# Optimization experiments

Measured on AMD Instinct MI355X. Metric: run time of the kernel, lower is better.

The kernel has to match this reference:

```python
import jax, jax.numpy as jnp
import numpy as np

B, N, M, D, F, H = 8, 512, 512, 512, 512, 8
D_H, F_H = D // H, F // H


def setup_inputs() -> dict:
    key = jax.random.key(0)
    ks = jax.random.split(key, 7)
    X = jax.random.normal(ks[0], (B, N, D), dtype=jnp.float32)
    V = jax.random.normal(ks[1], (B, M, F), dtype=jnp.float32)
    # learned parameters, init normal(0, 0.02) as in the torch module
    W_Q_1 = 0.02 * jax.random.normal(ks[2], (H, N, D_H, D_H), dtype=jnp.float32)
    W_Q_2 = 0.02 * jax.random.normal(ks[3], (H, N, M, D_H), dtype=jnp.float32)
    W_V = 0.02 * jax.random.normal(ks[4], (H, F_H, F_H), dtype=jnp.float32)
    O_w = 0.02 * jax.random.normal(ks[5], (F, F), dtype=jnp.float32)
    O_b = jnp.zeros((F,), dtype=jnp.float32)
    return {"X": X, "V": V, "W_Q_1": W_Q_1, "W_Q_2": W_Q_2,
            "W_V": W_V, "O_w": O_w, "O_b": O_b}


def reference(X, V, W_Q_1, W_Q_2, W_V, O_w, O_b):
    b, n, d = X.shape
    _, m, f = V.shape
    Xh = X.reshape(b, n, H, d // H)      # [B,N,H,D_H]
    Vh = V.reshape(b, m, H, f // H)      # [B,M,H,F_H]
    # 'hndd' repeats d within one operand -> diagonal of W_Q_1's last two dims
    # (faithful to torch.einsum semantics): per-position per-channel scale.
    Q_1 = jnp.einsum('bnhd,hndd->bhnd', Xh, W_Q_1)
    Q_1 = jax.nn.gelu(Q_1, approximate=False)  # torch nn.GELU default = exact erf
    Q_2 = jnp.einsum('bhnd,hnmd->bhnm', Q_1, W_Q_2)  # synthesized attention logits
    A = jax.nn.softmax(Q_2, axis=3)                  # softmax over M
    # 'hff' likewise takes the diagonal of W_V -> per-head channel scale fused
    # with the attention-weighted value aggregation.
    Y = jnp.einsum('bhnm,bmhf,hff->bnhf', A, Vh, W_V)
    Y = Y.reshape(b, n, f)
    return Y @ O_w.T + O_b
```

## Files before the change

### kernel.cpp

```cpp
#include <hip/hip_runtime.h>
#include <cstdint>

#define B_ 8
#define N_ 512
#define M_ 512
#define D_ 512
#define F_ 512
#define H_ 8
#define DH_ 64
#define FH_ 64

typedef __attribute__((ext_vector_type(8))) short bf16x8;
typedef __attribute__((ext_vector_type(4))) float f32x4;
typedef __attribute__((ext_vector_type(8))) unsigned short u16x8;

__device__ __forceinline__ unsigned short f2bf(float x) {
    unsigned u = __float_as_uint(x);
    return (unsigned short)((u + 0x7fffu + ((u >> 16) & 1u)) >> 16);
}
__device__ __forceinline__ float bf2f(unsigned short b) {
    return __uint_as_float(((unsigned)b) << 16);
}

template <int CTRL>
__device__ __forceinline__ float dpp_add(float x) {
    int y = __builtin_amdgcn_update_dpp(0, __float_as_int(x), CTRL, 0xf, 0xf, true);
    return x + __int_as_float(y);
}

__global__ __launch_bounds__(256, 4) void syn_k_attn(const float* __restrict__ X,
                                                     const float* __restrict__ W1,
                                                     const float* __restrict__ W2,
                                                     float* __restrict__ A) {
    int hn = blockIdx.x;
    int h = hn >> 9, n = hn & 511;
    int t = threadIdx.x;
    int wave = t >> 6, lane = t & 63;
    __shared__ float q1s[8 * 68];
    __shared__ float logits[8 * 520];

    {
        int d = t & 63;
        int b0 = t >> 6;
        float w = W1[(size_t)hn * (DH_ * DH_) + d * (DH_ + 1)];
        #pragma unroll
        for (int i = 0; i < 2; ++i) {
            int bi = b0 + i * 4;
            float x = X[((size_t)(bi * N_ + n)) * D_ + h * DH_ + d];
            float v = x * w;
            q1s[bi * 68 + d] = 0.5f * v * (1.0f + erff(v * 0.70710678118654752440f));
        }
    }
    __syncthreads();

    int mr = lane >> 3, c = lane & 7;
    float4 qa[8], qb[8];
    #pragma unroll
    for (int b = 0; b < 8; ++b) {
        qa[b] = *(const float4*)&q1s[b * 68 + c * 8];
        qb[b] = *(const float4*)&q1s[b * 68 + c * 8 + 4];
    }

    const float* w2 = W2 + (size_t)hn * ((size_t)M_ * DH_);
    #pragma unroll 4
    for (int g = 0; g < 16; ++g) {
        int m = (wave + g * 4) * 8 + mr;
        const float* wr = w2 + (size_t)m * DH_ + c * 8;
        float4 wa = *(const float4*)wr;
        float4 wb = *(const float4*)(wr + 4);
        float acc[8];
        #pragma unroll
        for (int b = 0; b < 8; ++b) {
            float a0 = wa.x * qa[b].x + wa.y * qa[b].y + wa.z * qa[b].z + wa.w * qa[b].w
                     + wb.x * qb[b].x + wb.y * qb[b].y + wb.z * qb[b].z + wb.w * qb[b].w;
            a0 = dpp_add<0xB1>(a0);
            a0 = dpp_add<0x4E>(a0);
            a0 = dpp_add<0x124>(a0);
            acc[b] = a0;
        }
        float lo = c == 0 ? acc[0] : c == 1 ? acc[1] : c == 2 ? acc[2] : acc[3];
        float hi = c == 0 ? acc[4] : c == 1 ? acc[5] : c == 2 ? acc[6] : acc[7];
        if (c < 4) {
            logits[c * 520 + m] = lo;
            logits[(c + 4) * 520 + m] = hi;
        }
    }
    __syncthreads();

    for (int bb = wave; bb < 8; bb += 4) {
        const float* lrow = &logits[bb * 520 + lane * 8];
        float4 va = *(const float4*)lrow;
        float4 vb = *(const float4*)(lrow + 4);
        float v[8] = {va.x, va.y, va.z, va.w, vb.x, vb.y, vb.z, vb.w};
        float mx = v[0];
        #pragma unroll
        for (int i = 1; i < 8; ++i) mx = fmaxf(mx, v[i]);
        #pragma unroll
        for (int s = 1; s < 64; s <<= 1) mx = fmaxf(mx, __shfl_xor(mx, s));
        float e[8]; float sum = 0.f;
        #pragma unroll
        for (int i = 0; i < 8; ++i) { e[i] = expf(v[i] - mx); sum += e[i]; }
        #pragma unroll
        for (int s = 1; s < 64; s <<= 1) sum += __shfl_xor(sum, s);
        float inv = 1.0f / sum;
        float* outp = A + ((size_t)(bb * H_ + h) * N_ + n) * M_ + lane * 8;
        float4 o0 = make_float4(e[0] * inv, e[1] * inv, e[2] * inv, e[3] * inv);
        float4 o1 = make_float4(e[4] * inv, e[5] * inv, e[6] * inv, e[7] * inv);
        *(float4*)outp = o0;
        *(float4*)(outp + 4) = o1;
    }
}

__global__ __launch_bounds__(256) void syn_k_splitw(const float* __restrict__ Ow,
                                                    unsigned short* __restrict__ Whi,
                                                    unsigned short* __restrict__ Wlo) {
    int i = (blockIdx.x * 256 + threadIdx.x) * 4;
    float4 v = *(const float4*)(Ow + i);
    float vv[4] = {v.x, v.y, v.z, v.w};
    unsigned short hb[4], lb[4];
    #pragma unroll
    for (int j = 0; j < 4; ++j) {
        hb[j] = f2bf(vv[j]);
        lb[j] = f2bf(vv[j] - bf2f(hb[j]));
    }
    uint2 hv, lv;
    hv.x = (unsigned)hb[0] | ((unsigned)hb[1] << 16);
    hv.y = (unsigned)hb[2] | ((unsigned)hb[3] << 16);
    lv.x = (unsigned)lb[0] | ((unsigned)lb[1] << 16);
    lv.y = (unsigned)lb[2] | ((unsigned)lb[3] << 16);
    *(uint2*)(Whi + i) = hv;
    *(uint2*)(Wlo + i) = lv;
}

__global__ __launch_bounds__(256) void syn_k_splitv(const float* __restrict__ V,
                                                    unsigned short* __restrict__ Vthi,
                                                    unsigned short* __restrict__ Vtlo) {
    int bh = blockIdx.x;
    int b = bh >> 3, h = bh & 7;
    int t = threadIdx.x;
    __shared__ float lds[64 * 68];
    for (int m0 = 0; m0 < M_; m0 += 64) {
        int m = t >> 2, fo = (t & 3) * 16;
        const float* src = V + ((size_t)(b * M_ + m0 + m)) * F_ + h * FH_ + fo;
        #pragma unroll
        for (int i = 0; i < 4; ++i)
            *(float4*)&lds[m * 68 + fo + i * 4] = *(const float4*)(src + i * 4);
        __syncthreads();
        int f = t >> 2, mo = (t & 3) * 16;
        unsigned short hb[16], lb[16];
        #pragma unroll
        for (int i = 0; i < 16; ++i) {
            float x = lds[(mo + i) * 68 + f];
            hb[i] = f2bf(x);
            lb[i] = f2bf(x - bf2f(hb[i]));
        }
        size_t base = ((size_t)(bh * 64 + f)) * 512 + m0 + mo;
        *(u16x8*)(Vthi + base) = *(u16x8*)hb;
        *(u16x8*)(Vthi + base + 8) = *(u16x8*)&hb[8];
        *(u16x8*)(Vtlo + base) = *(u16x8*)lb;
        *(u16x8*)(Vtlo + base + 8) = *(u16x8*)&lb[8];
        __syncthreads();
    }
}

__global__ __launch_bounds__(256) void syn_k_pv_mfma(const float* __restrict__ A,
                                                     const unsigned short* __restrict__ Vthi,
                                                     const unsigned short* __restrict__ Vtlo,
                                                     const float* __restrict__ WV,
                                                     unsigned short* __restrict__ Yhi,
                                                     unsigned short* __restrict__ Ylo) {
    int bh = blockIdx.y;
    int b = bh >> 3, h = bh & 7;
    int n0 = blockIdx.x * 64;
    int t = threadIdx.x;
    int lane = t & 63, wave = t >> 6;
    int wr = wave >> 1, wc = wave & 1;
    __shared__ __align__(16) unsigned short Alh[64 * 64], All[64 * 64];
    __shared__ __align__(16) unsigned short Blh[64 * 64], Bll[64 * 64];
    f32x4 acc[2][2];
    #pragma unroll
    for (int i = 0; i < 2; ++i)
        #pragma unroll
        for (int j = 0; j < 2; ++j) acc[i][j] = (f32x4){0.f, 0.f, 0.f, 0.f};

    int srow = t >> 3, skg = t & 7;
    int sslot = skg ^ (srow & 7);
    const float* Abase = A + ((size_t)bh * N_ + n0) * M_;
    const unsigned short* Vhb = Vthi + ((size_t)bh * 64) * 512;
    const unsigned short* Vlb = Vtlo + ((size_t)bh * 64) * 512;

    #pragma unroll 1
    for (int mb = 0; mb < 8; ++mb) {
        int m0 = mb * 64;
        #pragma unroll
        for (int rr = 0; rr < 2; ++rr) {
            int row = srow + rr * 32;
            const float* ap = Abase + (size_t)row * M_ + m0 + skg * 8;
            float4 x0 = *(const float4*)ap;
            float4 x1 = *(const float4*)(ap + 4);
            float xs[8] = {x0.x, x0.y, x0.z, x0.w, x1.x, x1.y, x1.z, x1.w};
            unsigned short hb[8], lb[8];
            #pragma unroll
            for (int i = 0; i < 8; ++i) {
                hb[i] = f2bf(xs[i]);
                lb[i] = f2bf(xs[i] - bf2f(hb[i]));
            }
            *(u16x8*)&Alh[row * 64 + sslot * 8] = *(u16x8*)hb;
            *(u16x8*)&All[row * 64 + sslot * 8] = *(u16x8*)lb;
            *(u16x8*)&Blh[row * 64 + sslot * 8] =
                *(const u16x8*)(Vhb + (size_t)row * 512 + m0 + skg * 8);
            *(u16x8*)&Bll[row * 64 + sslot * 8] =
                *(const u16x8*)(Vlb + (size_t)row * 512 + m0 + skg * 8);
        }
        __syncthreads();
        #pragma unroll
        for (int mg = 0; mg < 2; ++mg) {
            int kslot = (mg * 4 + (lane >> 4)) ^ (lane & 7);
            bf16x8 afh[2], afl[2], bfh[2], bfl[2];
            #pragma unroll
            for (int q = 0; q < 2; ++q) {
                int arow = wr * 32 + q * 16 + (lane & 15);
                afh[q] = *(const bf16x8*)&Alh[arow * 64 + kslot * 8];
                afl[q] = *(const bf16x8*)&All[arow * 64 + kslot * 8];
                int brow = wc * 32 + q * 16 + (lane & 15);
                bfh[q] = *(const bf16x8*)&Blh[brow * 64 + kslot * 8];
                bfl[q] = *(const bf16x8*)&Bll[brow * 64 + kslot * 8];
            }
            #pragma unroll
            for (int i = 0; i < 2; ++i)
                #pragma unroll
                for (int j = 0; j < 2; ++j) {
                    acc[i][j] = __builtin_amdgcn_mfma_f32_16x16x32_bf16(afh[i], bfh[j], acc[i][j], 0, 0, 0);
                    acc[i][j] = __builtin_amdgcn_mfma_f32_16x16x32_bf16(afh[i], bfl[j], acc[i][j], 0, 0, 0);
                    acc[i][j] = __builtin_amdgcn_mfma_f32_16x16x32_bf16(afl[i], bfh[j], acc[i][j], 0, 0, 0);
                }
        }
        __syncthreads();
    }

    int crow = n0 + wr * 32 + (lane >> 4) * 4;
    int ccol = wc * 32 + (lane & 15);
    #pragma unroll
    for (int j = 0; j < 2; ++j) {
        int f = ccol + j * 16;
        float s = WV[(size_t)h * (FH_ * FH_) + f * (FH_ + 1)];
        #pragma unroll
        for (int i = 0; i < 2; ++i)
            #pragma unroll
            for (int r = 0; r < 4; ++r) {
                int row = crow + i * 16 + r;
                float y = acc[i][j][r] * s;
                unsigned short hb = f2bf(y);
                unsigned short lb = f2bf(y - bf2f(hb));
                size_t base = ((size_t)(b * N_ + row)) * F_ + h * FH_ + f;
                Yhi[base] = hb;
                Ylo[base] = lb;
            }
    }
}

__global__ __launch_bounds__(256) void syn_k_out_mfma(const unsigned short* __restrict__ Yhi,
                                                      const unsigned short* __restrict__ Ylo,
                                                      const unsigned short* __restrict__ Whi,
                                                      const unsigned short* __restrict__ Wlo,
                                                      const float* __restrict__ Ob,
                                                      float* __restrict__ out) {
    int r0 = blockIdx.x * 64;
    int f0 = blockIdx.y * 64;
    int t = threadIdx.x;
    int lane = t & 63, wave = t >> 6;
    int wr = wave >> 1, wc = wave & 1;
    __shared__ __align__(16) unsigned short Alh[64 * 64], All[64 * 64];
    __shared__ __align__(16) unsigned short Blh[64 * 64], Bll[64 * 64];
    f32x4 acc[2][2];
    #pragma unroll
    for (int i = 0; i < 2; ++i)
        #pragma unroll
        for (int j = 0; j < 2; ++j) acc[i][j] = (f32x4){0.f, 0.f, 0.f, 0.f};

    int srow = t >> 3, skg = t & 7;
    int sslot = skg ^ (srow & 7);

    #pragma unroll 1
    for (int kb = 0; kb < 512; kb += 64) {
        #pragma unroll
        for (int rr = 0; rr < 2; ++rr) {
            int row = srow + rr * 32;
            size_t ya = (size_t)(r0 + row) * 512 + kb + skg * 8;
            size_t wa = (size_t)(f0 + row) * 512 + kb + skg * 8;
            *(u16x8*)&Alh[row * 64 + sslot * 8] = *(const u16x8*)(Yhi + ya);
            *(u16x8*)&All[row * 64 + sslot * 8] = *(const u16x8*)(Ylo + ya);
            *(u16x8*)&Blh[row * 64 + sslot * 8] = *(const u16x8*)(Whi + wa);
            *(u16x8*)&Bll[row * 64 + sslot * 8] = *(const u16x8*)(Wlo + wa);
        }
        __syncthreads();
        #pragma unroll
        for (int mg = 0; mg < 2; ++mg) {
            int kslot = (mg * 4 + (lane >> 4)) ^ (lane & 7);
            bf16x8 afh[2], afl[2], bfh[2], bfl[2];
            #pragma unroll
            for (int q = 0; q < 2; ++q) {
                int arow = wr * 32 + q * 16 + (lane & 15);
                afh[q] = *(const bf16x8*)&Alh[arow * 64 + kslot * 8];
                afl[q] = *(const bf16x8*)&All[arow * 64 + kslot * 8];
                int brow = wc * 32 + q * 16 + (lane & 15);
                bfh[q] = *(const bf16x8*)&Blh[brow * 64 + kslot * 8];
                bfl[q] = *(const bf16x8*)&Bll[brow * 64 + kslot * 8];
            }
            #pragma unroll
            for (int i = 0; i < 2; ++i)
                #pragma unroll
                for (int j = 0; j < 2; ++j) {
                    acc[i][j] = __builtin_amdgcn_mfma_f32_16x16x32_bf16(afh[i], bfh[j], acc[i][j], 0, 0, 0);
                    acc[i][j] = __builtin_amdgcn_mfma_f32_16x16x32_bf16(afh[i], bfl[j], acc[i][j], 0, 0, 0);
                    acc[i][j] = __builtin_amdgcn_mfma_f32_16x16x32_bf16(afl[i], bfh[j], acc[i][j], 0, 0, 0);
                }
        }
        __syncthreads();
    }

    int crow = r0 + wr * 32 + (lane >> 4) * 4;
    int ccol = f0 + wc * 32 + (lane & 15);
    float ob0 = Ob[ccol], ob1 = Ob[ccol + 16];
    #pragma unroll
    for (int i = 0; i < 2; ++i)
        #pragma unroll
        for (int j = 0; j < 2; ++j) {
            float obv = (j == 0) ? ob0 : ob1;
            #pragma unroll
            for (int r = 0; r < 4; ++r) {
                int row = crow + i * 16 + r;
                out[(size_t)row * F_ + ccol + j * 16] = acc[i][j][r] + obv;
            }
        }
}

extern "C" void kernel_launch(void* const* d_in, const int* in_sizes, int n_in,
                              void* d_out, int out_size, void* d_ws, size_t ws_size,
                              hipStream_t stream) {
    const float* X  = (const float*)d_in[0];
    const float* V  = (const float*)d_in[1];
    const float* W1 = (const float*)d_in[2];
    const float* W2 = (const float*)d_in[3];
    const float* WV = (const float*)d_in[4];
    const float* Ow = (const float*)d_in[5];
    const float* Ob = (const float*)d_in[6];
    float* out = (float*)d_out;

    float* ws = (float*)d_ws;
    float* A = ws;
    unsigned short* Yhi = (unsigned short*)(A + (size_t)B_ * H_ * N_ * M_);
    unsigned short* Ylo = Yhi + (size_t)B_ * N_ * F_;
    unsigned short* Whi = Ylo + (size_t)B_ * N_ * F_;
    unsigned short* Wlo = Whi + (size_t)F_ * F_;
    unsigned short* Vthi = Wlo + (size_t)F_ * F_;
    unsigned short* Vtlo = Vthi + (size_t)B_ * H_ * FH_ * M_;

    syn_k_splitw<<<(F_ * F_) / (256 * 4), 256, 0, stream>>>(Ow, Whi, Wlo);
    syn_k_splitv<<<B_ * H_, 256, 0, stream>>>(V, Vthi, Vtlo);
    syn_k_attn<<<H_ * N_, 256, 0, stream>>>(X, W1, W2, A);
    syn_k_pv_mfma<<<dim3(N_ / 64, B_ * H_), 256, 0, stream>>>(A, Vthi, Vtlo, WV, Yhi, Ylo);
    syn_k_out_mfma<<<dim3((B_ * N_) / 64, F_ / 64), 256, 0, stream>>>(Yhi, Ylo, Whi, Wlo, Ob, out);
}
```

Before: 190.7 us.

## Emit bf16 hi/lo attention from softmax, prefetch tiles, halve PV row tile

The softmax kernel now writes the attention matrix directly as bf16 hi/lo pairs instead of fp32, so the PV kernel no longer converts on load. The PV kernel uses 32-row tiles, doubling grid size for more parallelism, and prefetches the next K-tile into registers while computing the current one. The intermediate stays the same size in memory, but conversion work moves into the attention kernel and V tiles are reloaded by twice as many blocks.

```diff
diff --git a/kernel.cpp b/kernel.cpp
--- a/kernel.cpp
+++ b/kernel.cpp
@@ -31,7 +31,8 @@
 __global__ __launch_bounds__(256, 4) void syn_k_attn(const float* __restrict__ X,
                                                      const float* __restrict__ W1,
                                                      const float* __restrict__ W2,
-                                                     float* __restrict__ A) {
+                                                     unsigned short* __restrict__ Ahi,
+                                                     unsigned short* __restrict__ Alo) {
     int hn = blockIdx.x;
     int h = hn >> 9, n = hn & 511;
     int t = threadIdx.x;
@@ -103,11 +104,16 @@
         #pragma unroll
         for (int s = 1; s < 64; s <<= 1) sum += __shfl_xor(sum, s);
         float inv = 1.0f / sum;
-        float* outp = A + ((size_t)(bb * H_ + h) * N_ + n) * M_ + lane * 8;
-        float4 o0 = make_float4(e[0] * inv, e[1] * inv, e[2] * inv, e[3] * inv);
-        float4 o1 = make_float4(e[4] * inv, e[5] * inv, e[6] * inv, e[7] * inv);
-        *(float4*)outp = o0;
-        *(float4*)(outp + 4) = o1;
+        unsigned short hb[8], lb[8];
+        #pragma unroll
+        for (int i = 0; i < 8; ++i) {
+            float y = e[i] * inv;
+            hb[i] = f2bf(y);
+            lb[i] = f2bf(y - bf2f(hb[i]));
+        }
+        size_t base = ((size_t)(bb * H_ + h) * N_ + n) * M_ + lane * 8;
+        *(u16x8*)(Ahi + base) = *(u16x8*)hb;
+        *(u16x8*)(Alo + base) = *(u16x8*)lb;
     }
 }
 
@@ -163,7 +169,8 @@
     }
 }
 
-__global__ __launch_bounds__(256) void syn_k_pv_mfma(const float* __restrict__ A,
+__global__ __launch_bounds__(256) void syn_k_pv_mfma(const unsigned short* __restrict__ Ahi,
+                                                     const unsigned short* __restrict__ Alo,
                                                      const unsigned short* __restrict__ Vthi,
                                                      const unsigned short* __restrict__ Vtlo,
                                                      const float* __restrict__ WV,
@@ -171,91 +178,96 @@
                                                      unsigned short* __restrict__ Ylo) {
     int bh = blockIdx.y;
     int b = bh >> 3, h = bh & 7;
-    int n0 = blockIdx.x * 64;
+    int n0 = blockIdx.x * 32;
     int t = threadIdx.x;
     int lane = t & 63, wave = t >> 6;
     int wr = wave >> 1, wc = wave & 1;
-    __shared__ __align__(16) unsigned short Alh[64 * 64], All[64 * 64];
+    __shared__ __align__(16) unsigned short Alh[32 * 64], All[32 * 64];
     __shared__ __align__(16) unsigned short Blh[64 * 64], Bll[64 * 64];
-    f32x4 acc[2][2];
-    #pragma unroll
-    for (int i = 0; i < 2; ++i)
-        #pragma unroll
-        for (int j = 0; j < 2; ++j) acc[i][j] = (f32x4){0.f, 0.f, 0.f, 0.f};
+    f32x4 acc[2];
+    acc[0] = (f32x4){0.f, 0.f, 0.f, 0.f};
+    acc[1] = (f32x4){0.f, 0.f, 0.f, 0.f};
 
     int srow = t >> 3, skg = t & 7;
     int sslot = skg ^ (srow & 7);
-    const float* Abase = A + ((size_t)bh * N_ + n0) * M_;
+    const unsigned short* Ahb = Ahi + ((size_t)bh * N_ + n0) * M_;
+    const unsigned short* Alb = Alo + ((size_t)bh * N_ + n0) * M_;
     const unsigned short* Vhb = Vthi + ((size_t)bh * 64) * 512;
     const unsigned short* Vlb = Vtlo + ((size_t)bh * 64) * 512;
 
+    u16x8 rAh, rAl, rBh0, rBl0, rBh1, rBl1;
+    {
+        size_t aoff = (size_t)srow * M_ + skg * 8;
+        rAh = *(const u16x8*)(Ahb + aoff);
+        rAl = *(const u16x8*)(Alb + aoff);
+        size_t v0 = (size_t)srow * 512 + skg * 8;
+        size_t v1 = (size_t)(srow + 32) * 512 + skg * 8;
+        rBh0 = *(const u16x8*)(Vhb + v0);
+        rBl0 = *(const u16x8*)(Vlb + v0);
+        rBh1 = *(const u16x8*)(Vhb + v1);
+        rBl1 = *(const u16x8*)(Vlb + v1);
+    }
+
     #pragma unroll 1
     for (int mb = 0; mb < 8; ++mb) {
-        int m0 = mb * 64;
-        #pragma unroll
-        for (int rr = 0; rr < 2; ++rr) {
-            int row = srow + rr * 32;
-            const float* ap = Abase + (size_t)row * M_ + m0 + skg * 8;
-            float4 x0 = *(const float4*)ap;
-            float4 x1 = *(const float4*)(ap + 4);
-            float xs[8] = {x0.x, x0.y, x0.z, x0.w, x1.x, x1.y, x1.z, x1.w};
-            unsigned short hb[8], lb[8];
-            #pragma unroll
-            for (int i = 0; i < 8; ++i) {
-                hb[i] = f2bf(xs[i]);
-                lb[i] = f2bf(xs[i] - bf2f(hb[i]));
-            }
-            *(u16x8*)&Alh[row * 64 + sslot * 8] = *(u16x8*)hb;
-            *(u16x8*)&All[row * 64 + sslot * 8] = *(u16x8*)lb;
-            *(u16x8*)&Blh[row * 64 + sslot * 8] =
-                *(const u16x8*)(Vhb + (size_t)row * 512 + m0 + skg * 8);
-            *(u16x8*)&Bll[row * 64 + sslot * 8] =
-                *(const u16x8*)(Vlb + (size_t)row * 512 + m0 + skg * 8);
-        }
-        __syncthreads();
+        *(u16x8*)&Alh[srow * 64 + sslot * 8] = rAh;
+        *(u16x8*)&All[srow * 64 + sslot * 8] = rAl;
+        *(u16x8*)&Blh[srow * 64 + sslot * 8] = rBh0;
+        *(u16x8*)&Bll[srow * 64 + sslot * 8] = rBl0;
+        *(u16x8*)&Blh[(srow + 32) * 64 + sslot * 8] = rBh1;
+        *(u16x8*)&Bll[(srow + 32) * 64 + sslot * 8] = rBl1;
+        __syncthreads();
+        if (mb < 7) {
+            int m0 = (mb + 1) * 64;
+            size_t aoff = (size_t)srow * M_ + m0 + skg * 8;
+            rAh = *(const u16x8*)(Ahb + aoff);
+            rAl = *(const u16x8*)(Alb + aoff);
+            size_t v0 = (size_t)srow * 512 + m0 + skg * 8;
+            size_t v1 = (size_t)(srow + 32) * 512 + m0 + skg * 8;
+            rBh0 = *(const u16x8*)(Vhb + v0);
+            rBl0 = *(const u16x8*)(Vlb + v0);
+            rBh1 = *(const u16x8*)(Vhb + v1);
+            rBl1 = *(const u16x8*)(Vlb + v1);
+        }
         #pragma unroll
         for (int mg = 0; mg < 2; ++mg) {
             int kslot = (mg * 4 + (lane >> 4)) ^ (lane & 7);
-            bf16x8 afh[2], afl[2], bfh[2], bfl[2];
-            #pragma unroll
-            for (int q = 0; q < 2; ++q) {
-                int arow = wr * 32 + q * 16 + (lane & 15);
-                afh[q] = *(const bf16x8*)&Alh[arow * 64 + kslot * 8];
-                afl[q] = *(const bf16x8*)&All[arow * 64 + kslot * 8];
-                int brow = wc * 32 + q * 16 + (lane & 15);
-                bfh[q] = *(const bf16x8*)&Blh[brow * 64 + kslot * 8];
-                bfl[q] = *(const bf16x8*)&Bll[brow * 64 + kslot * 8];
+            int arow = wr * 16 + (lane & 15);
+            bf16x8 afh = *(const bf16x8*)&Alh[arow * 64 + kslot * 8];
+            bf16x8 afl = *(const bf16x8*)&All[arow * 64 + kslot * 8];
+            bf16x8 bfh[2], bfl[2];
+            #pragma unroll
+            for (int j = 0; j < 2; ++j) {
+                int brow = wc * 32 + j * 16 + (lane & 15);
+                bfh[j] = *(const bf16x8*)&Blh[brow * 64 + kslot * 8];
+                bfl[j] = *(const bf16x8*)&Bll[brow * 64 + kslot * 8];
             }
             #pragma unroll
-            for (int i = 0; i < 2; ++i)
-                #pragma unroll
-                for (int j = 0; j < 2; ++j) {
-                    acc[i][j] = __builtin_amdgcn_mfma_f32_16x16x32_bf16(afh[i], bfh[j], acc[i][j], 0, 0, 0);
-                    acc[i][j] = __builtin_amdgcn_mfma_f32_16x16x32_bf16(afh[i], bfl[j], acc[i][j], 0, 0, 0);
-                    acc[i][j] = __builtin_amdgcn_mfma_f32_16x16x32_bf16(afl[i], bfh[j], acc[i][j], 0, 0, 0);
-                }
-        }
-        __syncthreads();
-    }
-
-    int crow = n0 + wr * 32 + (lane >> 4) * 4;
+            for (int j = 0; j < 2; ++j) {
+                acc[j] = __builtin_amdgcn_mfma_f32_16x16x32_bf16(afh, bfh[j], acc[j], 0, 0, 0);
+                acc[j] = __builtin_amdgcn_mfma_f32_16x16x32_bf16(afh, bfl[j], acc[j], 0, 0, 0);
+                acc[j] = __builtin_amdgcn_mfma_f32_16x16x32_bf16(afl, bfh[j], acc[j], 0, 0, 0);
+            }
+        }
+        __syncthreads();
+    }
+
+    int crow = n0 + wr * 16 + (lane >> 4) * 4;
     int ccol = wc * 32 + (lane & 15);
     #pragma unroll
     for (int j = 0; j < 2; ++j) {
         int f = ccol + j * 16;
         float s = WV[(size_t)h * (FH_ * FH_) + f * (FH_ + 1)];
         #pragma unroll
-        for (int i = 0; i < 2; ++i)
-            #pragma unroll
-            for (int r = 0; r < 4; ++r) {
-                int row = crow + i * 16 + r;
-                float y = acc[i][j][r] * s;
-                unsigned short hb = f2bf(y);
-                unsigned short lb = f2bf(y - bf2f(hb));
-                size_t base = ((size_t)(b * N_ + row)) * F_ + h * FH_ + f;
-                Yhi[base] = hb;
-                Ylo[base] = lb;
-            }
+        for (int r = 0; r < 4; ++r) {
+            int row = crow + r;
+            float y = acc[j][r] * s;
+            unsigned short hb = f2bf(y);
+            unsigned short lb = f2bf(y - bf2f(hb));
+            size_t base = ((size_t)(b * N_ + row)) * F_ + h * FH_ + f;
+            Yhi[base] = hb;
+            Ylo[base] = lb;
+        }
     }
 }
 
@@ -347,9 +359,9 @@
     const float* Ob = (const float*)d_in[6];
     float* out = (float*)d_out;
 
-    float* ws = (float*)d_ws;
-    float* A = ws;
-    unsigned short* Yhi = (unsigned short*)(A + (size_t)B_ * H_ * N_ * M_);
+    unsigned short* Ahi = (unsigned short*)d_ws;
+    unsigned short* Alo = Ahi + (size_t)B_ * H_ * N_ * M_;
+    unsigned short* Yhi = Alo + (size_t)B_ * H_ * N_ * M_;
     unsigned short* Ylo = Yhi + (size_t)B_ * N_ * F_;
     unsigned short* Whi = Ylo + (size_t)B_ * N_ * F_;
     unsigned short* Wlo = Whi + (size_t)F_ * F_;
@@ -358,7 +370,7 @@
 
     syn_k_splitw<<<(F_ * F_) / (256 * 4), 256, 0, stream>>>(Ow, Whi, Wlo);
     syn_k_splitv<<<B_ * H_, 256, 0, stream>>>(V, Vthi, Vtlo);
-    syn_k_attn<<<H_ * N_, 256, 0, stream>>>(X, W1, W2, A);
-    syn_k_pv_mfma<<<dim3(N_ / 64, B_ * H_), 256, 0, stream>>>(A, Vthi, Vtlo, WV, Yhi, Ylo);
+    syn_k_attn<<<H_ * N_, 256, 0, stream>>>(X, W1, W2, Ahi, Alo);
+    syn_k_pv_mfma<<<dim3(N_ / 32, B_ * H_), 256, 0, stream>>>(Ahi, Alo, Vthi, Vtlo, WV, Yhi, Ylo);
     syn_k_out_mfma<<<dim3((B_ * N_) / 64, F_ / 64), 256, 0, stream>>>(Yhi, Ylo, Whi, Wlo, Ob, out);
 }
```

Measured after the change: 191.6 us. About the same (+0.5%).

## Fuse softmax and PV aggregation into the attention kernel, dropping the A buffer

Applied to the files above, without the earlier changes.

The attention kernel now handles two query positions per block. It normalises the logits in place in shared memory and immediately computes the attention-weighted sum over V with fp32 FMAs. It then writes the split-bf16 Y directly. This removes the large fp32 attention matrix round trip through global memory, the V transpose/split kernel and the separate MFMA PV kernel. The trade-off is that V is re-read from cache by every block and the PV product runs on scalar ALUs instead of matrix cores, which raises L2 traffic and VALU work.

```diff
diff --git a/kernel.cpp b/kernel.cpp
--- a/kernel.cpp
+++ b/kernel.cpp
@@ -9,6 +9,7 @@
 #define H_ 8
 #define DH_ 64
 #define FH_ 64
+#define NQ 2
 
 typedef __attribute__((ext_vector_type(8))) short bf16x8;
 typedef __attribute__((ext_vector_type(4))) float f32x4;
@@ -28,86 +29,152 @@
     return x + __int_as_float(y);
 }
 
-__global__ __launch_bounds__(256, 4) void syn_k_attn(const float* __restrict__ X,
-                                                     const float* __restrict__ W1,
-                                                     const float* __restrict__ W2,
-                                                     float* __restrict__ A) {
-    int hn = blockIdx.x;
-    int h = hn >> 9, n = hn & 511;
+__global__ __launch_bounds__(256, 4) void syn_k_attn_pv(const float* __restrict__ X,
+                                                        const float* __restrict__ W1,
+                                                        const float* __restrict__ W2,
+                                                        const float* __restrict__ V,
+                                                        const float* __restrict__ WV,
+                                                        unsigned short* __restrict__ Yhi,
+                                                        unsigned short* __restrict__ Ylo) {
+    int bid = blockIdx.x;
+    int h = bid & 7;
+    int n0 = (bid >> 3) * NQ;
     int t = threadIdx.x;
     int wave = t >> 6, lane = t & 63;
-    __shared__ float q1s[8 * 68];
-    __shared__ float logits[8 * 520];
-
-    {
+    __shared__ float q1s[NQ][8 * 68];
+    __shared__ float logits[NQ][8 * 520];
+
+    #pragma unroll
+    for (int nq = 0; nq < NQ; ++nq) {
+        int n = n0 + nq;
+        int hn = h * 512 + n;
         int d = t & 63;
         int b0 = t >> 6;
-        float w = W1[(size_t)hn * (DH_ * DH_) + d * (DH_ + 1)];
+        float w = W1[(size_t)hn * 4096 + d * 65];
         #pragma unroll
         for (int i = 0; i < 2; ++i) {
             int bi = b0 + i * 4;
             float x = X[((size_t)(bi * N_ + n)) * D_ + h * DH_ + d];
             float v = x * w;
-            q1s[bi * 68 + d] = 0.5f * v * (1.0f + erff(v * 0.70710678118654752440f));
+            q1s[nq][bi * 68 + d] = 0.5f * v * (1.0f + erff(v * 0.70710678118654752440f));
         }
     }
     __syncthreads();
 
     int mr = lane >> 3, c = lane & 7;
-    float4 qa[8], qb[8];
-    #pragma unroll
-    for (int b = 0; b < 8; ++b) {
-        qa[b] = *(const float4*)&q1s[b * 68 + c * 8];
-        qb[b] = *(const float4*)&q1s[b * 68 + c * 8 + 4];
-    }
-
-    const float* w2 = W2 + (size_t)hn * ((size_t)M_ * DH_);
-    #pragma unroll 4
-    for (int g = 0; g < 16; ++g) {
-        int m = (wave + g * 4) * 8 + mr;
-        const float* wr = w2 + (size_t)m * DH_ + c * 8;
-        float4 wa = *(const float4*)wr;
-        float4 wb = *(const float4*)(wr + 4);
-        float acc[8];
+    #pragma unroll 1
+    for (int nq = 0; nq < NQ; ++nq) {
+        int n = n0 + nq;
+        int hn = h * 512 + n;
+        float4 qa[8], qb[8];
         #pragma unroll
         for (int b = 0; b < 8; ++b) {
-            float a0 = wa.x * qa[b].x + wa.y * qa[b].y + wa.z * qa[b].z + wa.w * qa[b].w
-                     + wb.x * qb[b].x + wb.y * qb[b].y + wb.z * qb[b].z + wb.w * qb[b].w;
-            a0 = dpp_add<0xB1>(a0);
-            a0 = dpp_add<0x4E>(a0);
-            a0 = dpp_add<0x124>(a0);
-            acc[b] = a0;
-        }
-        float lo = c == 0 ? acc[0] : c == 1 ? acc[1] : c == 2 ? acc[2] : acc[3];
-        float hi = c == 0 ? acc[4] : c == 1 ? acc[5] : c == 2 ? acc[6] : acc[7];
-        if (c < 4) {
-            logits[c * 520 + m] = lo;
-            logits[(c + 4) * 520 + m] = hi;
+            qa[b] = *(const float4*)&q1s[nq][b * 68 + c * 8];
+            qb[b] = *(const float4*)&q1s[nq][b * 68 + c * 8 + 4];
+        }
+        const float* w2 = W2 + (size_t)hn * ((size_t)M_ * DH_);
+        #pragma unroll 4
+        for (int g = 0; g < 16; ++g) {
+            int m = (wave + g * 4) * 8 + mr;
+            const float* wr = w2 + (size_t)m * DH_ + c * 8;
+            float4 wa = *(const float4*)wr;
+            float4 wb = *(const float4*)(wr + 4);
+            float acc[8];
+            #pragma unroll
+            for (int b = 0; b < 8; ++b) {
+                float a0 = wa.x * qa[b].x + wa.y * qa[b].y + wa.z * qa[b].z + wa.w * qa[b].w
+                         + wb.x * qb[b].x + wb.y * qb[b].y + wb.z * qb[b].z + wb.w * qb[b].w;
+                a0 = dpp_add<0xB1>(a0);
+                a0 = dpp_add<0x4E>(a0);
+                a0 = dpp_add<0x124>(a0);
+                acc[b] = a0;
+            }
+            float lo = c == 0 ? acc[0] : c == 1 ? acc[1] : c == 2 ? acc[2] : acc[3];
+            float hi = c == 0 ? acc[4] : c == 1 ? acc[5] : c == 2 ? acc[6] : acc[7];
+            if (c < 4) {
+                logits[nq][c * 520 + m] = lo;
+                logits[nq][(c + 4) * 520 + m] = hi;
+            }
         }
     }
     __syncthreads();
 
+    int ms = lane >> 3, fg = lane & 7;
+    float wv[8];
+    #pragma unroll
+    for (int j = 0; j < 8; ++j)
+        wv[j] = WV[(size_t)h * 4096 + (fg * 8 + j) * 65];
+
+    #pragma unroll 1
     for (int bb = wave; bb < 8; bb += 4) {
-        const float* lrow = &logits[bb * 520 + lane * 8];
-        float4 va = *(const float4*)lrow;
-        float4 vb = *(const float4*)(lrow + 4);
-        float v[8] = {va.x, va.y, va.z, va.w, vb.x, vb.y, vb.z, vb.w};
-        float mx = v[0];
-        #pragma unroll
-        for (int i = 1; i < 8; ++i) mx = fmaxf(mx, v[i]);
-        #pragma unroll
-        for (int s = 1; s < 64; s <<= 1) mx = fmaxf(mx, __shfl_xor(mx, s));
-        float e[8]; float sum = 0.f;
-        #pragma unroll
-        for (int i = 0; i < 8; ++i) { e[i] = expf(v[i] - mx); sum += e[i]; }
-        #pragma unroll
-        for (int s = 1; s < 64; s <<= 1) sum += __shfl_xor(sum, s);
-        float inv = 1.0f / sum;
-        float* outp = A + ((size_t)(bb * H_ + h) * N_ + n) * M_ + lane * 8;
-        float4 o0 = make_float4(e[0] * inv, e[1] * inv, e[2] * inv, e[3] * inv);
-        float4 o1 = make_float4(e[4] * inv, e[5] * inv, e[6] * inv, e[7] * inv);
-        *(float4*)outp = o0;
-        *(float4*)(outp + 4) = o1;
+        #pragma unroll
+        for (int nq = 0; nq < NQ; ++nq) {
+            float* lrow = &logits[nq][bb * 520];
+            float4 va = *(const float4*)(lrow + lane * 8);
+            float4 vb = *(const float4*)(lrow + lane * 8 + 4);
+            float v[8] = {va.x, va.y, va.z, va.w, vb.x, vb.y, vb.z, vb.w};
+            float mx = v[0];
+            #pragma unroll
+            for (int i = 1; i < 8; ++i) mx = fmaxf(mx, v[i]);
+            #pragma unroll
+            for (int s = 1; s < 64; s <<= 1) mx = fmaxf(mx, __shfl_xor(mx, s));
+            float e[8]; float sum = 0.f;
+            #pragma unroll
+            for (int i = 0; i < 8; ++i) { e[i] = expf(v[i] - mx); sum += e[i]; }
+            #pragma unroll
+            for (int s = 1; s < 64; s <<= 1) sum += __shfl_xor(sum, s);
+            float inv = 1.0f / sum;
+            float4 o0 = make_float4(e[0] * inv, e[1] * inv, e[2] * inv, e[3] * inv);
+            float4 o1 = make_float4(e[4] * inv, e[5] * inv, e[6] * inv, e[7] * inv);
+            *(float4*)(lrow + lane * 8) = o0;
+            *(float4*)(lrow + lane * 8 + 4) = o1;
+        }
+
+        float acc0[8] = {0.f, 0.f, 0.f, 0.f, 0.f, 0.f, 0.f, 0.f};
+        float acc1[8] = {0.f, 0.f, 0.f, 0.f, 0.f, 0.f, 0.f, 0.f};
+        const float* vbase = V + ((size_t)(bb * M_ + ms)) * F_ + h * FH_ + fg * 8;
+        const float* l0 = &logits[0][bb * 520];
+        const float* l1 = &logits[1][bb * 520];
+        #pragma unroll 4
+        for (int m0 = 0; m0 < 512; m0 += 8) {
+            const float* vp = vbase + (size_t)m0 * F_;
+            float4 v0 = *(const float4*)vp;
+            float4 v1 = *(const float4*)(vp + 4);
+            float e0 = l0[m0 + ms];
+            float e1 = l1[m0 + ms];
+            float vv[8] = {v0.x, v0.y, v0.z, v0.w, v1.x, v1.y, v1.z, v1.w};
+            #pragma unroll
+            for (int j = 0; j < 8; ++j) {
+                acc0[j] += e0 * vv[j];
+                acc1[j] += e1 * vv[j];
+            }
+        }
+        #pragma unroll
+        for (int j = 0; j < 8; ++j) {
+            acc0[j] += __shfl_xor(acc0[j], 8);
+            acc0[j] += __shfl_xor(acc0[j], 16);
+            acc0[j] += __shfl_xor(acc0[j], 32);
+            acc1[j] += __shfl_xor(acc1[j], 8);
+            acc1[j] += __shfl_xor(acc1[j], 16);
+            acc1[j] += __shfl_xor(acc1[j], 32);
+        }
+        if (ms == 0) {
+            unsigned short hb0[8], lb0[8], hb1[8], lb1[8];
+            #pragma unroll
+            for (int j = 0; j < 8; ++j) {
+                float y0 = acc0[j] * wv[j];
+                hb0[j] = f2bf(y0);
+                lb0[j] = f2bf(y0 - bf2f(hb0[j]));
+                float y1 = acc1[j] * wv[j];
+                hb1[j] = f2bf(y1);
+                lb1[j] = f2bf(y1 - bf2f(hb1[j]));
+            }
+            size_t yb = ((size_t)(bb * N_ + n0)) * F_ + h * FH_ + fg * 8;
+            *(u16x8*)(Yhi + yb) = *(u16x8*)hb0;
+            *(u16x8*)(Ylo + yb) = *(u16x8*)lb0;
+            *(u16x8*)(Yhi + yb + F_) = *(u16x8*)hb1;
+            *(u16x8*)(Ylo + yb + F_) = *(u16x8*)lb1;
+        }
     }
 }
 
@@ -130,133 +197,6 @@
     lv.y = (unsigned)lb[2] | ((unsigned)lb[3] << 16);
     *(uint2*)(Whi + i) = hv;
     *(uint2*)(Wlo + i) = lv;
-}
-
-__global__ __launch_bounds__(256) void syn_k_splitv(const float* __restrict__ V,
-                                                    unsigned short* __restrict__ Vthi,
-                                                    unsigned short* __restrict__ Vtlo) {
-    int bh = blockIdx.x;
-    int b = bh >> 3, h = bh & 7;
-    int t = threadIdx.x;
-    __shared__ float lds[64 * 68];
-    for (int m0 = 0; m0 < M_; m0 += 64) {
-        int m = t >> 2, fo = (t & 3) * 16;
-        const float* src = V + ((size_t)(b * M_ + m0 + m)) * F_ + h * FH_ + fo;
-        #pragma unroll
-        for (int i = 0; i < 4; ++i)
-            *(float4*)&lds[m * 68 + fo + i * 4] = *(const float4*)(src + i * 4);
-        __syncthreads();
-        int f = t >> 2, mo = (t & 3) * 16;
-        unsigned short hb[16], lb[16];
-        #pragma unroll
-        for (int i = 0; i < 16; ++i) {
-            float x = lds[(mo + i) * 68 + f];
-            hb[i] = f2bf(x);
-            lb[i] = f2bf(x - bf2f(hb[i]));
-        }
-        size_t base = ((size_t)(bh * 64 + f)) * 512 + m0 + mo;
-        *(u16x8*)(Vthi + base) = *(u16x8*)hb;
-        *(u16x8*)(Vthi + base + 8) = *(u16x8*)&hb[8];
-        *(u16x8*)(Vtlo + base) = *(u16x8*)lb;
-        *(u16x8*)(Vtlo + base + 8) = *(u16x8*)&lb[8];
-        __syncthreads();
-    }
-}
-
-__global__ __launch_bounds__(256) void syn_k_pv_mfma(const float* __restrict__ A,
-                                                     const unsigned short* __restrict__ Vthi,
-                                                     const unsigned short* __restrict__ Vtlo,
-                                                     const float* __restrict__ WV,
-                                                     unsigned short* __restrict__ Yhi,
-                                                     unsigned short* __restrict__ Ylo) {
-    int bh = blockIdx.y;
-    int b = bh >> 3, h = bh & 7;
-    int n0 = blockIdx.x * 64;
-    int t = threadIdx.x;
-    int lane = t & 63, wave = t >> 6;
-    int wr = wave >> 1, wc = wave & 1;
-    __shared__ __align__(16) unsigned short Alh[64 * 64], All[64 * 64];
-    __shared__ __align__(16) unsigned short Blh[64 * 64], Bll[64 * 64];
-    f32x4 acc[2][2];
-    #pragma unroll
-    for (int i = 0; i < 2; ++i)
-        #pragma unroll
-        for (int j = 0; j < 2; ++j) acc[i][j] = (f32x4){0.f, 0.f, 0.f, 0.f};
-
-    int srow = t >> 3, skg = t & 7;
-    int sslot = skg ^ (srow & 7);
-    const float* Abase = A + ((size_t)bh * N_ + n0) * M_;
-    const unsigned short* Vhb = Vthi + ((size_t)bh * 64) * 512;
-    const unsigned short* Vlb = Vtlo + ((size_t)bh * 64) * 512;
-
-    #pragma unroll 1
-    for (int mb = 0; mb < 8; ++mb) {
-        int m0 = mb * 64;
-        #pragma unroll
-        for (int rr = 0; rr < 2; ++rr) {
-            int row = srow + rr * 32;
-            const float* ap = Abase + (size_t)row * M_ + m0 + skg * 8;
-            float4 x0 = *(const float4*)ap;
-            float4 x1 = *(const float4*)(ap + 4);
-            float xs[8] = {x0.x, x0.y, x0.z, x0.w, x1.x, x1.y, x1.z, x1.w};
-            unsigned short hb[8], lb[8];
-            #pragma unroll
-            for (int i = 0; i < 8; ++i) {
-                hb[i] = f2bf(xs[i]);
-                lb[i] = f2bf(xs[i] - bf2f(hb[i]));
-            }
-            *(u16x8*)&Alh[row * 64 + sslot * 8] = *(u16x8*)hb;
-            *(u16x8*)&All[row * 64 + sslot * 8] = *(u16x8*)lb;
-            *(u16x8*)&Blh[row * 64 + sslot * 8] =
-                *(const u16x8*)(Vhb + (size_t)row * 512 + m0 + skg * 8);
-            *(u16x8*)&Bll[row * 64 + sslot * 8] =
-                *(const u16x8*)(Vlb + (size_t)row * 512 + m0 + skg * 8);
-        }
-        __syncthreads();
-        #pragma unroll
-        for (int mg = 0; mg < 2; ++mg) {
-            int kslot = (mg * 4 + (lane >> 4)) ^ (lane & 7);
-            bf16x8 afh[2], afl[2], bfh[2], bfl[2];
-            #pragma unroll
-            for (int q = 0; q < 2; ++q) {
-                int arow = wr * 32 + q * 16 + (lane & 15);
-                afh[q] = *(const bf16x8*)&Alh[arow * 64 + kslot * 8];
-                afl[q] = *(const bf16x8*)&All[arow * 64 + kslot * 8];
-                int brow = wc * 32 + q * 16 + (lane & 15);
-                bfh[q] = *(const bf16x8*)&Blh[brow * 64 + kslot * 8];
-                bfl[q] = *(const bf16x8*)&Bll[brow * 64 + kslot * 8];
-            }
-            #pragma unroll
-            for (int i = 0; i < 2; ++i)
-                #pragma unroll
-                for (int j = 0; j < 2; ++j) {
-                    acc[i][j] = __builtin_amdgcn_mfma_f32_16x16x32_bf16(afh[i], bfh[j], acc[i][j], 0, 0, 0);
-                    acc[i][j] = __builtin_amdgcn_mfma_f32_16x16x32_bf16(afh[i], bfl[j], acc[i][j], 0, 0, 0);
-                    acc[i][j] = __builtin_amdgcn_mfma_f32_16x16x32_bf16(afl[i], bfh[j], acc[i][j], 0, 0, 0);
-                }
-        }
-        __syncthreads();
-    }
-
-    int crow = n0 + wr * 32 + (lane >> 4) * 4;
-    int ccol = wc * 32 + (lane & 15);
-    #pragma unroll
-    for (int j = 0; j < 2; ++j) {
-        int f = ccol + j * 16;
-        float s = WV[(size_t)h * (FH_ * FH_) + f * (FH_ + 1)];
-        #pragma unroll
-        for (int i = 0; i < 2; ++i)
-            #pragma unroll
-            for (int r = 0; r < 4; ++r) {
-                int row = crow + i * 16 + r;
-                float y = acc[i][j][r] * s;
-                unsigned short hb = f2bf(y);
-                unsigned short lb = f2bf(y - bf2f(hb));
-                size_t base = ((size_t)(b * N_ + row)) * F_ + h * FH_ + f;
-                Yhi[base] = hb;
-                Ylo[base] = lb;
-            }
-    }
 }
 
 __global__ __launch_bounds__(256) void syn_k_out_mfma(const unsigned short* __restrict__ Yhi,
@@ -347,18 +287,12 @@
     const float* Ob = (const float*)d_in[6];
     float* out = (float*)d_out;
 
-    float* ws = (float*)d_ws;
-    float* A = ws;
-    unsigned short* Yhi = (unsigned short*)(A + (size_t)B_ * H_ * N_ * M_);
+    unsigned short* Yhi = (unsigned short*)d_ws;
     unsigned short* Ylo = Yhi + (size_t)B_ * N_ * F_;
     unsigned short* Whi = Ylo + (size_t)B_ * N_ * F_;
     unsigned short* Wlo = Whi + (size_t)F_ * F_;
-    unsigned short* Vthi = Wlo + (size_t)F_ * F_;
-    unsigned short* Vtlo = Vthi + (size_t)B_ * H_ * FH_ * M_;
 
     syn_k_splitw<<<(F_ * F_) / (256 * 4), 256, 0, stream>>>(Ow, Whi, Wlo);
-    syn_k_splitv<<<B_ * H_, 256, 0, stream>>>(V, Vthi, Vtlo);
-    syn_k_attn<<<H_ * N_, 256, 0, stream>>>(X, W1, W2, A);
-    syn_k_pv_mfma<<<dim3(N_ / 64, B_ * H_), 256, 0, stream>>>(A, Vthi, Vtlo, WV, Yhi, Ylo);
+    syn_k_attn_pv<<<(H_ * N_) / NQ, 256, 0, stream>>>(X, W1, W2, V, WV, Yhi, Ylo);
     syn_k_out_mfma<<<dim3((B_ * N_) / 64, F_ / 64), 256, 0, stream>>>(Yhi, Ylo, Whi, Wlo, Ob, out);
 }
```

New measurement: 230.9 us. +21.1%, slower.
